# Kernel tuning notes

Hardware: AMD Instinct MI355X
Metric: run time of the kernel (lower is better)

The kernel has to match this reference:

```python
import jax, jax.numpy as jnp
import numpy as np

B, N, CIN, C = 2, 400000, 192, 128
Y, X, Z = 512, 512, 40
EPS1 = 1e-5   # default BatchNorm1d eps for feature_proj
EPS2 = 1e-3   # norm_fn eps=0.001 for shared_conv BN


def setup_inputs() -> dict:
    key = jax.random.key(0)
    ks = jax.random.split(key, 12)
    voxel_features = jax.random.normal(ks[0], (N, CIN), jnp.float32)
    bi = jax.random.randint(ks[1], (N,), 0, B)
    zi = jax.random.randint(ks[2], (N,), 0, Z)
    yi = jax.random.randint(ks[3], (N,), 0, Y)
    xi = jax.random.randint(ks[4], (N,), 0, X)
    voxel_coords = jnp.stack([bi, zi, yi, xi], axis=1).astype(jnp.int32)  # (N,4)=[b,z,y,x]
    # feature_proj: Linear(CIN->C) + BN1d (inference stats) + ReLU
    W_proj = jax.random.normal(ks[5], (CIN, C), jnp.float32) * np.float32(1.0 / np.sqrt(CIN))
    b_proj = jnp.zeros((C,), jnp.float32)
    bn1_gamma = jnp.ones((C,), jnp.float32)
    bn1_beta = jnp.zeros((C,), jnp.float32)
    bn1_mean = jax.random.normal(ks[6], (C,), jnp.float32) * np.float32(0.1)
    bn1_var = jax.random.uniform(ks[7], (C,), jnp.float32, 0.5, 1.5)
    # shared_conv: SubMConv2d(C,C,3,pad=1,bias) + BN(eps=1e-3) + ReLU
    conv_w = jax.random.normal(ks[8], (3, 3, C, C), jnp.float32) * np.float32(1.0 / np.sqrt(9 * C))
    conv_b = jnp.zeros((C,), jnp.float32)
    bn2_gamma = jnp.ones((C,), jnp.float32)
    bn2_beta = jnp.zeros((C,), jnp.float32)
    bn2_mean = jax.random.normal(ks[9], (C,), jnp.float32) * np.float32(0.1)
    bn2_var = jax.random.uniform(ks[10], (C,), jnp.float32, 0.5, 1.5)
    return dict(voxel_features=voxel_features, voxel_coords=voxel_coords,
                W_proj=W_proj, b_proj=b_proj,
                bn1_gamma=bn1_gamma, bn1_beta=bn1_beta, bn1_mean=bn1_mean, bn1_var=bn1_var,
                conv_w=conv_w, conv_b=conv_b,
                bn2_gamma=bn2_gamma, bn2_beta=bn2_beta, bn2_mean=bn2_mean, bn2_var=bn2_var)


def reference(voxel_features, voxel_coords, W_proj, b_proj,
              bn1_gamma, bn1_beta, bn1_mean, bn1_var,
              conv_w, conv_b, bn2_gamma, bn2_beta, bn2_mean, bn2_var):
    # 1) feature_proj (Linear + BN1d inference + ReLU)
    f = voxel_features @ W_proj + b_proj                      # (N, C)
    f = (f - bn1_mean) * jax.lax.rsqrt(bn1_var + EPS1) * bn1_gamma + bn1_beta
    f = jax.nn.relu(f)
    # 2) bev_aggregate: unique([b,y,x]) + index_add == scatter-sum to dense BEV grid
    bi, yi, xi = voxel_coords[:, 0], voxel_coords[:, 2], voxel_coords[:, 3]
    dense = jnp.zeros((B, Y, X, C), f.dtype).at[bi, yi, xi].add(f)
    active = jnp.zeros((B, Y, X), bool).at[bi, yi, xi].set(True)
    # 3) SubMConv2d(3x3, pad=1) + BN + ReLU; subm == dense conv masked to active sites
    out = jax.lax.conv_general_dilated(dense, conv_w, (1, 1), 'SAME',
                                       dimension_numbers=('NHWC', 'HWIO', 'NHWC')) + conv_b
    out = (out - bn2_mean) * jax.lax.rsqrt(bn2_var + EPS2) * bn2_gamma + bn2_beta
    out = jax.nn.relu(out)
    # sparse tensor only holds active sites; zero elsewhere
    return jnp.where(active[..., None], out, jnp.float32(0.0))  # (B, Y, X, C)
```

## Files before the change

kernel.cpp:

```cpp
#include <hip/hip_runtime.h>

#define Bq 2
#define Yq 512
#define Xq 512

typedef __bf16 bf16x8 __attribute__((ext_vector_type(8)));
typedef float f32x4 __attribute__((ext_vector_type(4)));
typedef float f32x16 __attribute__((ext_vector_type(16)));
typedef short s16x8 __attribute__((ext_vector_type(8)));
typedef short s16x2 __attribute__((ext_vector_type(2)));

__device__ __forceinline__ short f2bf_s(float f){
    return __builtin_bit_cast(short, static_cast<__bf16>(f));
}
__device__ __forceinline__ float bfbits2f(unsigned short u){
    unsigned v = ((unsigned)u) << 16; return __builtin_bit_cast(float, v);
}

__device__ __forceinline__ void atomic_pk_add_bf16(short* addr, short lo, short hi){
#if __has_builtin(__builtin_amdgcn_global_atomic_fadd_v2bf16)
    s16x2 v; v[0] = lo; v[1] = hi;
    __builtin_amdgcn_global_atomic_fadd_v2bf16(
        (__attribute__((address_space(1))) s16x2*)addr, v);
#else
    unsigned* p = (unsigned*)addr;
    float flo = bfbits2f((unsigned short)lo), fhi = bfbits2f((unsigned short)hi);
    unsigned old = *p, seen;
    do {
        seen = old;
        unsigned short olo = (unsigned short)(seen & 0xffff);
        unsigned short ohi = (unsigned short)(seen >> 16);
        unsigned short nlo = (unsigned short)f2bf_s(bfbits2f(olo) + flo);
        unsigned short nhi = (unsigned short)f2bf_s(bfbits2f(ohi) + fhi);
        unsigned nv = ((unsigned)nhi << 16) | nlo;
        old = atomicCAS(p, seen, nv);
    } while (old != seen);
#endif
}

__global__ void kprep(const float* __restrict__ conv_w, const float* __restrict__ W_proj,
                      short* __restrict__ wTs, short* __restrict__ wpT){
    int tid = blockIdx.x*256 + threadIdx.x;
    if (tid < 9*128*128){
        int tap = tid >> 14; int r = tid & 16383; int co = r >> 7; int ci = r & 127;
        int g = ci >> 3, e = ci & 7;
        wTs[tap*16384 + co*128 + (((g & 8) | ((g & 7) ^ (co & 7))) << 3) + e] =
            f2bf_s(conv_w[tap*16384 + ci*128 + co]);
    }
    int e = tid - 9*128*128;
    if (e >= 0 && e < 128*192){
        int co = e / 192; int ci = e - co*192;
        wpT[e] = f2bf_s(W_proj[ci*128 + co]);
    }
}

__global__ void __launch_bounds__(256, 2)
kproj(const float* __restrict__ vf, const int* __restrict__ vc,
      const short* __restrict__ wpT, const float* __restrict__ bp,
      const float* __restrict__ g1, const float* __restrict__ be1,
      const float* __restrict__ mu1, const float* __restrict__ va1,
      short* __restrict__ dbf, unsigned char* __restrict__ act){
    __shared__ short A[64*200];
    __shared__ int cellsPk[64];
    const int t = threadIdx.x;
    const int v0 = blockIdx.x * 64;

    const float4* vf4 = reinterpret_cast<const float4*>(vf);
    #pragma unroll
    for (int j = 0; j < 12; ++j){
        int i = t + j*256;
        int v = i / 48, kq = i - v*48;
        float4 x = vf4[(size_t)(v0 + v)*48 + kq];
        short4 s; s.x=f2bf_s(x.x); s.y=f2bf_s(x.y); s.z=f2bf_s(x.z); s.w=f2bf_s(x.w);
        *reinterpret_cast<short4*>(&A[v*200 + kq*4]) = s;
    }
    if (t < 64){
        int vi = v0 + t;
        int bi = vc[vi*4 + 0], yi = vc[vi*4 + 2], xi = vc[vi*4 + 3];
        act[(bi*Yq + yi)*Xq + xi] = 1;
        int P = (bi*514 + (yi + 1))*514 + (xi + 1);
        cellsPk[t] = P*8 + ((xi + 1) & 7);
    }
    __syncthreads();

    const int w  = t >> 6;
    const int l  = t & 63;
    const int lr = l & 15;
    const int q  = l >> 4;

    const short* wp_lane = wpT + (size_t)(w*32 + lr)*192 + q*8;
    bf16x8 bb[2][6];
    #pragma unroll
    for (int n = 0; n < 2; ++n)
        #pragma unroll
        for (int kc = 0; kc < 6; ++kc)
            bb[n][kc] = *reinterpret_cast<const bf16x8*>(wp_lane + n*16*192 + kc*32);

    f32x4 acc[4][2] = {};
    #pragma unroll
    for (int kc = 0; kc < 6; ++kc){
        bf16x8 a[4];
        #pragma unroll
        for (int m = 0; m < 4; ++m)
            a[m] = *reinterpret_cast<const bf16x8*>(&A[(m*16 + lr)*200 + kc*32 + q*8]);
        #pragma unroll
        for (int m = 0; m < 4; ++m)
            #pragma unroll
            for (int n = 0; n < 2; ++n)
                acc[m][n] = __builtin_amdgcn_mfma_f32_16x16x32_bf16(a[m], bb[n][kc], acc[m][n], 0, 0, 0);
    }

    #pragma unroll
    for (int n = 0; n < 2; ++n){
        int c = w*32 + n*16 + lr;
        float s1  = g1[c] * rsqrtf(va1[c] + 1e-5f);
        float sh1 = be1[c] + (bp[c] - mu1[c]) * s1;
        #pragma unroll
        for (int m = 0; m < 4; ++m){
            #pragma unroll
            for (int r = 0; r < 4; ++r){
                int vx = m*16 + q*4 + r;
                float val = fmaxf(fmaf(acc[m][n][r], s1, sh1), 0.f);
                float vp  = __shfl_xor(val, 1);
                if ((lr & 1) == 0 && (val != 0.f || vp != 0.f)){
                    int pk = cellsPk[vx];
                    int P = pk >> 3, xp7 = pk & 7;
                    short* addr = dbf + (size_t)P*128 + (((c >> 3) ^ xp7) << 3) + (c & 7);
                    atomic_pk_add_bf16(addr, f2bf_s(val), f2bf_s(vp));
                }
            }
        }
    }
}

__global__ void __launch_bounds__(512, 2)
kconv(const short* __restrict__ dbf, const short* __restrict__ wTs,
      const unsigned char* __restrict__ act, const float* __restrict__ cb,
      const float* __restrict__ g2, const float* __restrict__ be2,
      const float* __restrict__ mu2, const float* __restrict__ va2,
      float* __restrict__ out){
    __shared__ short Atile[6*1056*8];
    __shared__ short Bbuf[2][1024*8];
    const int t = threadIdx.x;
    const int bid = (blockIdx.x & 7)*256 + (blockIdx.x >> 3);
    const int b   = bid >> 10;
    const int rem = bid & 1023;
    const int y0  = (rem >> 3) << 2;
    const int x0  = (rem & 7) << 6;

    const int w   = t >> 6, l = t & 63;
    const int yy  = w >> 1, nn = w & 1;
    const int l31 = l & 31, hi = l >> 5;
    const int wbase16 = w*64*16;

    #define STAGE_B(BUF, H) do {                                              \
        const short* gb = wTs + (size_t)((H) >> 1)*16384 + ((H) & 1)*64;      \
        _Pragma("unroll")                                                     \
        for (int j = 0; j < 2; ++j){                                          \
            int S = j*512 + t;                                                \
            const short* gp = gb + (S >> 3)*128 + (S & 7)*8;                  \
            __builtin_amdgcn_global_load_lds(                                 \
                (const __attribute__((address_space(1))) void*)gp,            \
                (__attribute__((address_space(3))) void*)                    \
                    ((char*)Bbuf[BUF] + (size_t)(j*512*16) + wbase16), 16, 0, 0); \
        }                                                                     \
    } while(0)

    STAGE_B(0, 0);
    #pragma unroll
    for (int j = 0; j < 13; ++j){
        int S = j*512 + t;
        if (S < 6336){
            int r = S / 1056, s = S - r*1056;
            const short* gp = dbf + ((size_t)((b*514 + (y0 + r))*514 + x0)*16 + s)*8;
            __builtin_amdgcn_global_load_lds(
                (const __attribute__((address_space(1))) void*)gp,
                (__attribute__((address_space(3))) void*)
                    ((char*)Atile + (size_t)(j*512*16) + wbase16), 16, 0, 0);
        }
    }
    __syncthreads();

    f32x16 acc[2][2] = {};
    const int bReadBase = (nn*64 + l31)*64;
    const int bXor = l31 & 7;

    #pragma unroll
    for (int h = 0; h < 18; ++h){
        if (h < 17) STAGE_B((h+1) & 1, h+1);
        const short* Bc = Bbuf[h & 1];
        const int tap = h >> 1, hh = h & 1;
        const int ky = tap / 3, kx = tap - ky*3;
        const int row = yy + ky;
        const int p0 = l31 + kx, p1 = p0 + 32;
        const int base0 = (row*1056 + p0*16)*8;
        const int base1 = (row*1056 + p1*16)*8;
        const int pk7 = p0 & 7;
        #pragma unroll
        for (int kc = 0; kc < 4; ++kc){
            const int ks  = kc*2 + hi;
            const int q   = ((hh*8 + ks) ^ pk7) << 3;
            const int qb  = (ks ^ bXor) << 3;
            bf16x8 a0 = *reinterpret_cast<const bf16x8*>(&Atile[base0 + q]);
            bf16x8 a1 = *reinterpret_cast<const bf16x8*>(&Atile[base1 + q]);
            bf16x8 b0 = *reinterpret_cast<const bf16x8*>(&Bc[bReadBase + qb]);
            bf16x8 b1 = *reinterpret_cast<const bf16x8*>(&Bc[bReadBase + 2048 + qb]);
            acc[0][0] = __builtin_amdgcn_mfma_f32_32x32x16_bf16(a0, b0, acc[0][0], 0, 0, 0);
            acc[0][1] = __builtin_amdgcn_mfma_f32_32x32x16_bf16(a0, b1, acc[0][1], 0, 0, 0);
            acc[1][0] = __builtin_amdgcn_mfma_f32_32x32x16_bf16(a1, b0, acc[1][0], 0, 0, 0);
            acc[1][1] = __builtin_amdgcn_mfma_f32_32x32x16_bf16(a1, b1, acc[1][1], 0, 0, 0);
        }
        __syncthreads();
    }
    #undef STAGE_B

    const int yg = y0 + yy;
    const size_t rowcell = (size_t)(b*Yq + yg)*Xq + x0;
    #pragma unroll
    for (int ni = 0; ni < 2; ++ni){
        int c = nn*64 + ni*32 + l31;
        float s2  = g2[c] * rsqrtf(va2[c] + 1e-3f);
        float sh2 = be2[c] + (cb[c] - mu2[c]) * s2;
        #pragma unroll
        for (int mi = 0; mi < 2; ++mi){
            #pragma unroll
            for (int r = 0; r < 16; ++r){
                int pos = mi*32 + (r & 3) + ((r >> 2) << 3) + hi*4;
                size_t cell = rowcell + pos;
                float v = act[cell] ? fmaxf(fmaf(acc[mi][ni][r], s2, sh2), 0.f) : 0.f;
                out[cell*128 + c] = v;
            }
        }
    }
}

extern "C" void kernel_launch(void* const* d_in, const int* in_sizes, int n_in,
                              void* d_out, int out_size, void* d_ws, size_t ws_size,
                              hipStream_t stream){
    const float* vf  = (const float*)d_in[0];
    const int*   vc  = (const int*)  d_in[1];
    const float* Wp  = (const float*)d_in[2];
    const float* bp  = (const float*)d_in[3];
    const float* g1  = (const float*)d_in[4];
    const float* be1 = (const float*)d_in[5];
    const float* mu1 = (const float*)d_in[6];
    const float* va1 = (const float*)d_in[7];
    const float* cw  = (const float*)d_in[8];
    const float* cb  = (const float*)d_in[9];
    const float* g2  = (const float*)d_in[10];
    const float* be2 = (const float*)d_in[11];
    const float* mu2 = (const float*)d_in[12];
    const float* va2 = (const float*)d_in[13];
    float* out = (float*)d_out;
    char* ws = (char*)d_ws;

    if (ws_size < 136136704ull) return;
    short* dbf = (short*)ws;
    unsigned char* act = (unsigned char*)(ws + 135268352);
    short* wTs = (short*)(ws + 135792640);
    short* wpT = (short*)(ws + 136087552);

    hipMemsetAsync(dbf, 0, 135268352, stream);
    hipMemsetAsync(act, 0, 524288, stream);
    kprep<<<672, 256, 0, stream>>>(cw, Wp, wTs, wpT);
    kproj<<<6250, 256, 0, stream>>>(vf, vc, wpT, bp, g1, be1, mu1, va1, dbf, act);
    kconv<<<2048, 512, 0, stream>>>(dbf, wTs, act, cb, g2, be2, mu2, va2, out);
}
```

Measured before the change: 426.5 us.

## Count voxels per cell and use plain stores for singly-occupied cells

```diff
diff --git a/kernel.cpp b/kernel.cpp
--- a/kernel.cpp
+++ b/kernel.cpp
@@ -3,6 +3,7 @@
 #define Bq 2
 #define Yq 512
 #define Xq 512
+#define NVOX 400000
 
 typedef __bf16 bf16x8 __attribute__((ext_vector_type(8)));
 typedef float f32x4 __attribute__((ext_vector_type(4)));
@@ -13,28 +14,15 @@
 __device__ __forceinline__ short f2bf_s(float f){
     return __builtin_bit_cast(short, static_cast<__bf16>(f));
 }
-__device__ __forceinline__ float bfbits2f(unsigned short u){
-    unsigned v = ((unsigned)u) << 16; return __builtin_bit_cast(float, v);
-}
-
-__device__ __forceinline__ void atomic_pk_add_bf16(short* addr, short lo, short hi){
+
+__device__ __forceinline__ void atomic_pk_add_bf16(short* addr, unsigned data){
 #if __has_builtin(__builtin_amdgcn_global_atomic_fadd_v2bf16)
-    s16x2 v; v[0] = lo; v[1] = hi;
+    s16x2 v; v[0] = (short)(data & 0xffff); v[1] = (short)(data >> 16);
     __builtin_amdgcn_global_atomic_fadd_v2bf16(
         (__attribute__((address_space(1))) s16x2*)addr, v);
 #else
-    unsigned* p = (unsigned*)addr;
-    float flo = bfbits2f((unsigned short)lo), fhi = bfbits2f((unsigned short)hi);
-    unsigned old = *p, seen;
-    do {
-        seen = old;
-        unsigned short olo = (unsigned short)(seen & 0xffff);
-        unsigned short ohi = (unsigned short)(seen >> 16);
-        unsigned short nlo = (unsigned short)f2bf_s(bfbits2f(olo) + flo);
-        unsigned short nhi = (unsigned short)f2bf_s(bfbits2f(ohi) + fhi);
-        unsigned nv = ((unsigned)nhi << 16) | nlo;
-        old = atomicCAS(p, seen, nv);
-    } while (old != seen);
+    asm volatile("global_atomic_pk_add_bf16 %0, %1, off"
+                 :: "v"(addr), "v"(data) : "memory");
 #endif
 }
 
@@ -54,12 +42,23 @@
     }
 }
 
+__global__ void kcount(const int* __restrict__ vc, unsigned* __restrict__ cnt,
+                       unsigned char* __restrict__ act){
+    int i = blockIdx.x*256 + threadIdx.x;
+    if (i >= NVOX) return;
+    const int4 c = *reinterpret_cast<const int4*>(vc + i*4);
+    int cell = (c.x*Yq + c.z)*Xq + c.w;
+    act[cell] = 1;
+    atomicAdd(&cnt[cell], 1u);
+}
+
 __global__ void __launch_bounds__(256, 2)
 kproj(const float* __restrict__ vf, const int* __restrict__ vc,
+      const unsigned* __restrict__ cnt,
       const short* __restrict__ wpT, const float* __restrict__ bp,
       const float* __restrict__ g1, const float* __restrict__ be1,
       const float* __restrict__ mu1, const float* __restrict__ va1,
-      short* __restrict__ dbf, unsigned char* __restrict__ act){
+      short* __restrict__ dbf){
     __shared__ short A[64*200];
     __shared__ int cellsPk[64];
     const int t = threadIdx.x;
@@ -77,9 +76,9 @@
     if (t < 64){
         int vi = v0 + t;
         int bi = vc[vi*4 + 0], yi = vc[vi*4 + 2], xi = vc[vi*4 + 3];
-        act[(bi*Yq + yi)*Xq + xi] = 1;
+        unsigned cn = cnt[(bi*Yq + yi)*Xq + xi];
         int P = (bi*514 + (yi + 1))*514 + (xi + 1);
-        cellsPk[t] = P*8 + ((xi + 1) & 7);
+        cellsPk[t] = (P*8 + ((xi + 1) & 7)) | ((cn > 1) ? (1 << 30) : 0);
     }
     __syncthreads();
 
@@ -122,11 +121,18 @@
                 int vx = m*16 + q*4 + r;
                 float val = fmaxf(fmaf(acc[m][n][r], s1, sh1), 0.f);
                 float vp  = __shfl_xor(val, 1);
-                if ((lr & 1) == 0 && (val != 0.f || vp != 0.f)){
+                if ((lr & 1) == 0){
                     int pk = cellsPk[vx];
-                    int P = pk >> 3, xp7 = pk & 7;
+                    int multi = pk >> 30;
+                    int P = (pk & 0x3fffffff) >> 3, xp7 = pk & 7;
                     short* addr = dbf + (size_t)P*128 + (((c >> 3) ^ xp7) << 3) + (c & 7);
-                    atomic_pk_add_bf16(addr, f2bf_s(val), f2bf_s(vp));
+                    unsigned data = (unsigned)(unsigned short)f2bf_s(val)
+                                  | ((unsigned)(unsigned short)f2bf_s(vp) << 16);
+                    if (!multi){
+                        if (data) *reinterpret_cast<unsigned*>(addr) = data;
+                    } else {
+                        if (data) atomic_pk_add_bf16(addr, data);
+                    }
                 }
             }
         }
@@ -254,15 +260,18 @@
     float* out = (float*)d_out;
     char* ws = (char*)d_ws;
 
-    if (ws_size < 136136704ull) return;
+    if (ws_size < 138233856ull) return;
     short* dbf = (short*)ws;
     unsigned char* act = (unsigned char*)(ws + 135268352);
     short* wTs = (short*)(ws + 135792640);
     short* wpT = (short*)(ws + 136087552);
+    unsigned* cnt = (unsigned*)(ws + 136136704);
 
     hipMemsetAsync(dbf, 0, 135268352, stream);
     hipMemsetAsync(act, 0, 524288, stream);
+    hipMemsetAsync(cnt, 0, 2097152, stream);
     kprep<<<672, 256, 0, stream>>>(cw, Wp, wTs, wpT);
-    kproj<<<6250, 256, 0, stream>>>(vf, vc, wpT, bp, g1, be1, mu1, va1, dbf, act);
+    kcount<<<1563, 256, 0, stream>>>(vc, cnt, act);
+    kproj<<<6250, 256, 0, stream>>>(vf, vc, cnt, wpT, bp, g1, be1, mu1, va1, dbf);
     kconv<<<2048, 512, 0, stream>>>(dbf, wTs, act, cb, g2, be2, mu2, va2, out);
 }
```

Measured after the change: 402.7 us. -5.6%, faster.
